# Kernel tuning notes

Hardware: AMD Instinct MI355X
Metric: run time of the kernel (lower is better)

## Reference

```python
import jax, jax.numpy as jnp
import numpy as np
from jax import lax

D_MODEL = 768
N_LAYER = 4
VOCAB = 50280  # 50277 padded to multiple of 8
D_INNER = 2 * D_MODEL
D_STATE = 16
D_CONV = 4
DT_RANK = 48  # ceil(768/16)
EPS = 1e-5


def setup_inputs() -> dict:
    key = jax.random.key(0)
    ks = iter(jax.random.split(key, 16))
    s = 0.02
    B, L = 1, 1024
    inp = {
        "input_ids": jax.random.randint(next(ks), (B, L), 0, 50277, dtype=jnp.int64).astype(jnp.int32),
        "embedding": jax.random.normal(next(ks), (VOCAB, D_MODEL), jnp.float32) * s,
        "in_proj_w": jax.random.normal(next(ks), (N_LAYER, 2 * D_INNER, D_MODEL), jnp.float32) * s,
        "conv_w": jax.random.normal(next(ks), (N_LAYER, D_INNER, 1, D_CONV), jnp.float32) * s,
        "conv_b": jnp.zeros((N_LAYER, D_INNER), jnp.float32),
        "x_proj_w": jax.random.normal(next(ks), (N_LAYER, DT_RANK + 2 * D_STATE, D_INNER), jnp.float32) * s,
        "dt_proj_w": jax.random.normal(next(ks), (N_LAYER, D_INNER, DT_RANK), jnp.float32) * s,
        "dt_proj_b": jax.random.uniform(next(ks), (N_LAYER, D_INNER), jnp.float32, -4.0, -2.0),
        "A_log": jnp.log(jnp.broadcast_to(jnp.arange(1, D_STATE + 1, dtype=jnp.float32), (N_LAYER, D_INNER, D_STATE))),
        "D_param": jnp.ones((N_LAYER, D_INNER), jnp.float32),
        "out_proj_w": jax.random.normal(next(ks), (N_LAYER, D_MODEL, D_INNER), jnp.float32) * s,
        "norm_w": jnp.ones((N_LAYER, D_MODEL), jnp.float32),
        "norm_f_w": jnp.ones((D_MODEL,), jnp.float32),
    }
    return inp


def rmsnorm(x, w):
    var = jnp.mean(jnp.square(x), axis=-1, keepdims=True)
    return x * lax.rsqrt(var + EPS) * w


def silu(x):
    return x * jax.nn.sigmoid(x)


def mamba_mixer(h, in_w, cw, cb, xw, dtw, dtb, A_log, Dp, ow):
    B, L, _ = h.shape
    xz = jnp.einsum("bld,ed->ble", h, in_w)          # [B,L,2*d_inner]
    x, z = jnp.split(xz, 2, axis=-1)
    # causal depthwise conv1d over length
    xc = lax.conv_general_dilated(
        x.transpose(0, 2, 1), cw, (1,), [(D_CONV - 1, 0)],
        dimension_numbers=("NCH", "OIH", "NCH"), feature_group_count=D_INNER,
    ).transpose(0, 2, 1) + cb                          # [B,L,d_inner]
    xc = silu(xc)
    dbl = jnp.einsum("bld,ed->ble", xc, xw)            # [B,L,R+2N]
    dt = jax.nn.softplus(jnp.einsum("blr,dr->bld", dbl[..., :DT_RANK], dtw) + dtb)
    Bm = dbl[..., DT_RANK:DT_RANK + D_STATE]           # [B,L,N]
    Cm = dbl[..., DT_RANK + D_STATE:]                  # [B,L,N]
    A = -jnp.exp(A_log)                                # [d_inner,N]
    dA = jnp.exp(dt[..., None] * A)                    # [B,L,d_inner,N]
    dBx = dt[..., None] * Bm[:, :, None, :] * xc[..., None]

    def step(s, inp):
        a, b, c = inp
        s = a * s + b
        y = jnp.einsum("bdn,bn->bd", s, c)
        return s, y

    s0 = jnp.zeros((B, D_INNER, D_STATE), h.dtype)
    _, ys = lax.scan(step, s0, (dA.transpose(1, 0, 2, 3), dBx.transpose(1, 0, 2, 3), Cm.transpose(1, 0, 2)))
    y = ys.transpose(1, 0, 2) + xc * Dp                # [B,L,d_inner]
    y = y * silu(z)
    return jnp.einsum("ble,de->bld", y, ow)


def reference(input_ids, embedding, in_proj_w, conv_w, conv_b, x_proj_w,
              dt_proj_w, dt_proj_b, A_log, D_param, out_proj_w, norm_w, norm_f_w):
    h = embedding[input_ids]                           # [B,L,D]
    for i in range(N_LAYER):
        h = h + mamba_mixer(rmsnorm(h, norm_w[i]), in_proj_w[i], conv_w[i], conv_b[i],
                            x_proj_w[i], dt_proj_w[i], dt_proj_b[i], A_log[i],
                            D_param[i], out_proj_w[i])
    h = rmsnorm(h, norm_f_w)
    logits = jnp.einsum("bld,vd->blv", h, embedding)   # tied lm_head
    return logits
```

## Files before the change

### kernel.cpp

```cpp
#include <hip/hip_runtime.h>
#include <cstdint>
#include <cstddef>

#define N_LAYER 4
#define VOCABSZ 50280
#define VOCABPAD 50304
#define DMODEL 768
#define DINNER 1536
#define DSTATE 16
#define DTRANK 48
#define SEQL 1024
#define HPSTRIDE (SEQL * DMODEL)
#define XPSTRIDE (SEQL * 80)

typedef __bf16 bf16x8 __attribute__((ext_vector_type(8)));
typedef unsigned short us8 __attribute__((ext_vector_type(8)));
typedef float f32x4 __attribute__((ext_vector_type(4)));

__device__ __forceinline__ unsigned short f2bf(float f) {
    unsigned int u = __builtin_bit_cast(unsigned int, f);
    u = (u + 0x7FFFu + ((u >> 16) & 1u)) >> 16;
    return (unsigned short)u;
}

__device__ __forceinline__ void glds16(const unsigned short* g, unsigned short* l) {
    __builtin_amdgcn_global_load_lds(
        (const __attribute__((address_space(1))) void*)g,
        (__attribute__((address_space(3))) void*)l, 16, 0, 0);
}

__device__ __forceinline__ void cvt8(const float* s, unsigned short* d) {
    const float4* s4 = (const float4*)s;
    float4 a = s4[0], b = s4[1];
    us8 o = { f2bf(a.x), f2bf(a.y), f2bf(a.z), f2bf(a.w),
              f2bf(b.x), f2bf(b.y), f2bf(b.z), f2bf(b.w) };
    *(us8*)d = o;
}

__global__ __launch_bounds__(256) void cvt_bf16_kernel(
    const float* __restrict__ src, unsigned short* __restrict__ dst, int n8)
{
    int i = blockIdx.x * 256 + threadIdx.x;
    if (i >= n8) return;
    cvt8(src + (size_t)i * 8, dst + (size_t)i * 8);
}

__global__ __launch_bounds__(256) void cvt3_kernel(
    const float* __restrict__ s0, unsigned short* __restrict__ d0, int n0,
    const float* __restrict__ s1, unsigned short* __restrict__ d1, int n1,
    const float* __restrict__ s2, unsigned short* __restrict__ d2, int n2)
{
    int i = blockIdx.x * 256 + threadIdx.x;
    const float* s; unsigned short* d; int j = i;
    if (j < n0) { s = s0; d = d0; }
    else {
        j -= n0;
        if (j < n1) { s = s1; d = d1; }
        else {
            j -= n1;
            if (j >= n2) return;
            s = s2; d = d2;
        }
    }
    cvt8(s + (size_t)j * 8, d + (size_t)j * 8);
}

__global__ __launch_bounds__(256) void cvt_xw_kernel(
    const float* __restrict__ xw, unsigned short* __restrict__ xwB)
{
    int g = blockIdx.x * 256 + threadIdx.x;
    if (g >= N_LAYER * 128 * 192) return;
    int row = g / 192;
    int c8  = g % 192;
    int layer = row >> 7;
    int r = row & 127;
    us8 o;
    if (r < 80) {
        const float4* s = (const float4*)(xw + ((size_t)(layer * 80 + r) * DINNER) + c8 * 8);
        float4 a = s[0], b = s[1];
        o = (us8){ f2bf(a.x), f2bf(a.y), f2bf(a.z), f2bf(a.w),
                   f2bf(b.x), f2bf(b.y), f2bf(b.z), f2bf(b.w) };
    } else {
        o = (us8){0, 0, 0, 0, 0, 0, 0, 0};
    }
    *(us8*)(xwB + (size_t)row * DINNER + c8 * 8) = o;
}

__device__ __forceinline__ void gemm_compute32(
    const unsigned short* sAbuf, const unsigned short* sBbuf,
    int wm, int wn, int frs, f32x4 (&acc)[4][4])
{
    bf16x8 af[4], bfr[4];
#pragma unroll
    for (int t = 0; t < 4; ++t) {
        af[t]  = __builtin_bit_cast(bf16x8, *(const us8*)&sAbuf[(wm + t * 16) * 32 + frs]);
        bfr[t] = __builtin_bit_cast(bf16x8, *(const us8*)&sBbuf[(wn + t * 16) * 32 + frs]);
    }
#pragma unroll
    for (int mt = 0; mt < 4; ++mt)
#pragma unroll
        for (int nt = 0; nt < 4; ++nt)
            acc[mt][nt] = __builtin_amdgcn_mfma_f32_16x16x32_bf16(
                af[mt], bfr[nt], acc[mt][nt], 0, 0, 0);
}

__device__ __forceinline__ void gemm_core(
    const unsigned short* __restrict__ A, const unsigned short* __restrict__ B,
    float* __restrict__ C, int N, int Kstride, int Klen, int bm, int bn)
{
    __shared__ unsigned short sA0[128 * 32];
    __shared__ unsigned short sA1[128 * 32];
    __shared__ unsigned short sB0[128 * 32];
    __shared__ unsigned short sB1[128 * 32];

    const int tid  = threadIdx.x;
    const int lane = tid & 63;
    const int wave = tid >> 6;
    const int wm = (wave & 1) * 64;
    const int wn = (wave >> 1) * 64;

    const int scol = ((tid & 3) ^ ((tid >> 3) & 3)) * 8;
    const unsigned short* Ag0 = A + (size_t)(bm + (tid >> 2)) * Kstride + scol;
    const unsigned short* Ag1 = Ag0 + (size_t)64 * Kstride;
    const unsigned short* Bg0 = B + (size_t)(bn + (tid >> 2)) * Kstride + scol;
    const unsigned short* Bg1 = Bg0 + (size_t)64 * Kstride;
    unsigned short* lA0a = sA0 + tid * 8;  unsigned short* lA0b = lA0a + 2048;
    unsigned short* lA1a = sA1 + tid * 8;  unsigned short* lA1b = lA1a + 2048;
    unsigned short* lB0a = sB0 + tid * 8;  unsigned short* lB0b = lB0a + 2048;
    unsigned short* lB1a = sB1 + tid * 8;  unsigned short* lB1b = lB1a + 2048;

    f32x4 acc[4][4];
#pragma unroll
    for (int i = 0; i < 4; ++i)
#pragma unroll
        for (int j = 0; j < 4; ++j) acc[i][j] = (f32x4){0.f, 0.f, 0.f, 0.f};

    const int frs = (lane & 15) * 32 + (((lane >> 4) ^ ((lane >> 1) & 3))) * 8;

    glds16(Ag0, lA0a); glds16(Ag1, lA0b);
    glds16(Bg0, lB0a); glds16(Bg1, lB0b);
    Ag0 += 32; Ag1 += 32; Bg0 += 32; Bg1 += 32;
    __syncthreads();

    for (int k0 = 0; k0 < Klen; k0 += 64) {
        glds16(Ag0, lA1a); glds16(Ag1, lA1b);
        glds16(Bg0, lB1a); glds16(Bg1, lB1b);
        Ag0 += 32; Ag1 += 32; Bg0 += 32; Bg1 += 32;
        gemm_compute32(sA0, sB0, wm, wn, frs, acc);
        __syncthreads();

        if (k0 + 64 < Klen) {
            glds16(Ag0, lA0a); glds16(Ag1, lA0b);
            glds16(Bg0, lB0a); glds16(Bg1, lB0b);
            Ag0 += 32; Ag1 += 32; Bg0 += 32; Bg1 += 32;
        }
        gemm_compute32(sA1, sB1, wm, wn, frs, acc);
        __syncthreads();
    }

    const int cn = lane & 15;
    const int cm = (lane >> 4) * 4;
#pragma unroll
    for (int mt = 0; mt < 4; ++mt) {
#pragma unroll
        for (int nt = 0; nt < 4; ++nt) {
            int n = bn + wn + nt * 16 + cn;
            if (n < N) {
#pragma unroll
                for (int r = 0; r < 4; ++r) {
                    int m = bm + wm + mt * 16 + cm + r;
                    C[(size_t)m * N + n] = acc[mt][nt][r];
                }
            }
        }
    }
}

__device__ __forceinline__ void swz_mn(int bid, int grid, int& bm, int& bn)
{
    int cpx = grid >> 3;
    int swz = (bid & 7) * cpx + (bid >> 3);
    bm = (swz & 7) << 7;
    bn = (swz >> 3) << 7;
}

__global__ __launch_bounds__(256) void gemm_in_kernel(
    const unsigned short* __restrict__ A, const unsigned short* __restrict__ B,
    float* __restrict__ C, int N, int K)
{ int bm, bn; swz_mn(blockIdx.x, gridDim.x, bm, bn); gemm_core(A, B, C, N, K, K, bm, bn); }

__global__ __launch_bounds__(256) void gemm_xprojk_kernel(
    const unsigned short* __restrict__ A, const unsigned short* __restrict__ B,
    float* __restrict__ xpp)
{
    int split = blockIdx.x >> 3;
    int bm = (blockIdx.x & 7) << 7;
    int kbase = split * 192;
    gemm_core(A + kbase, B + kbase, xpp + (size_t)split * XPSTRIDE,
              80, DINNER, 192, bm, 0);
}

__global__ __launch_bounds__(256) void xred_kernel(
    const float* __restrict__ xpp, float* __restrict__ dbl)
{
    int i = blockIdx.x * 256 + threadIdx.x;
    if (i >= XPSTRIDE / 4) return;
    const f32x4* p = (const f32x4*)xpp + i;
    f32x4 s = p[0];
#pragma unroll
    for (int k = 1; k < 8; ++k) s += p[(size_t)k * (XPSTRIDE / 4)];
    ((f32x4*)dbl)[i] = s;
}

__global__ __launch_bounds__(256) void gemm_outp_kernel(
    const unsigned short* __restrict__ A, const unsigned short* __restrict__ B,
    float* __restrict__ hp, int N, int Kstride, int Klen)
{
    int bid = blockIdx.x;
    int split = bid / 48;
    int r = bid - split * 48;
    int swz = (r & 7) * 6 + (r >> 3);
    int bm = (swz & 7) << 7;
    int bn = (swz >> 3) << 7;
    int kbase = split * Klen;
    gemm_core(A + kbase, B + kbase, hp + (size_t)split * HPSTRIDE,
              N, Kstride, Klen, bm, bn);
}

__global__ __launch_bounds__(256) void gemm_logits_kernel(
    const unsigned short* __restrict__ A, const unsigned short* __restrict__ B,
    float* __restrict__ C, int N, int K)
{
    __shared__ unsigned short sA[128 * 32];
    __shared__ unsigned short sB[128 * 32];

    const int tid  = threadIdx.x;
    const int lane = tid & 63;
    const int wave = tid >> 6;
    const int wm = (wave & 1) * 64;
    const int wn = (wave >> 1) * 64;
    int bm, bn;
    swz_mn(blockIdx.x, gridDim.x, bm, bn);

    const int scol = ((tid & 3) ^ ((tid >> 3) & 3)) * 8;
    const unsigned short* Ag0 = A + (size_t)(bm + (tid >> 2)) * K + scol;
    const unsigned short* Ag1 = Ag0 + (size_t)64 * K;
    const unsigned short* Bg0 = B + (size_t)(bn + (tid >> 2)) * K + scol;
    const unsigned short* Bg1 = Bg0 + (size_t)64 * K;
    unsigned short* lA0 = sA + tid * 8;
    unsigned short* lA1 = lA0 + 2048;
    unsigned short* lB0 = sB + tid * 8;
    unsigned short* lB1 = lB0 + 2048;

    f32x4 acc[4][4];
#pragma unroll
    for (int i = 0; i < 4; ++i)
#pragma unroll
        for (int j = 0; j < 4; ++j) acc[i][j] = (f32x4){0.f, 0.f, 0.f, 0.f};

    const int frs = (lane & 15) * 32 + (((lane >> 4) ^ ((lane >> 1) & 3))) * 8;

    for (int k0 = 0; k0 < K; k0 += 32) {
        __syncthreads();
        glds16(Ag0, lA0);
        glds16(Ag1, lA1);
        glds16(Bg0, lB0);
        glds16(Bg1, lB1);
        Ag0 += 32; Ag1 += 32; Bg0 += 32; Bg1 += 32;
        __syncthreads();
        gemm_compute32(sA, sB, wm, wn, frs, acc);
    }

    const int cn = lane & 15;
    const int cm = (lane >> 4) * 4;
#pragma unroll
    for (int mt = 0; mt < 4; ++mt) {
#pragma unroll
        for (int nt = 0; nt < 4; ++nt) {
            int n = bn + wn + nt * 16 + cn;
            if (n < N) {
#pragma unroll
                for (int r = 0; r < 4; ++r) {
                    int m = bm + wm + mt * 16 + cm + r;
                    C[(size_t)m * N + n] = acc[mt][nt][r];
                }
            }
        }
    }
}

template <int ADD>
__global__ __launch_bounds__(256) void gemm_fb_kernel(
    const float* __restrict__ A, const float* __restrict__ B,
    const float* __restrict__ ADDSRC, float* __restrict__ C,
    int N, int K)
{
    __shared__ unsigned short sA[128 * 40];
    __shared__ unsigned short sB[128 * 40];
    const int tid  = threadIdx.x;
    const int lane = tid & 63;
    const int wave = tid >> 6;
    const int wm = (wave & 1) * 64;
    const int wn = (wave >> 1) * 64;
    const int bm = blockIdx.y * 128;
    const int bn = blockIdx.x * 128;
    const int srow = tid >> 1;
    const int scol = (tid & 1) * 16;
    const float* Ap = A + (size_t)(bm + srow) * K + scol;
    const int brow  = bn + srow;
    const bool bvalid = brow < N;
    const float* Bp = B + (size_t)(bvalid ? brow : 0) * K + scol;
    f32x4 acc[4][4];
#pragma unroll
    for (int i = 0; i < 4; ++i)
#pragma unroll
        for (int j = 0; j < 4; ++j) acc[i][j] = (f32x4){0.f, 0.f, 0.f, 0.f};
    unsigned short* sAp = &sA[srow * 40 + scol];
    unsigned short* sBp = &sB[srow * 40 + scol];
    const int fr = (lane & 15) * 40 + (lane >> 4) * 8;
    for (int k0 = 0; k0 < K; k0 += 32) {
        float4 a0 = *(const float4*)(Ap + k0);
        float4 a1 = *(const float4*)(Ap + k0 + 4);
        float4 a2 = *(const float4*)(Ap + k0 + 8);
        float4 a3 = *(const float4*)(Ap + k0 + 12);
        float4 b0, b1, b2, b3;
        if (bvalid) {
            b0 = *(const float4*)(Bp + k0);
            b1 = *(const float4*)(Bp + k0 + 4);
            b2 = *(const float4*)(Bp + k0 + 8);
            b3 = *(const float4*)(Bp + k0 + 12);
        } else {
            b0 = make_float4(0.f, 0.f, 0.f, 0.f);
            b1 = b0; b2 = b0; b3 = b0;
        }
        __syncthreads();
        us8 va0 = { f2bf(a0.x), f2bf(a0.y), f2bf(a0.z), f2bf(a0.w),
                    f2bf(a1.x), f2bf(a1.y), f2bf(a1.z), f2bf(a1.w) };
        us8 va1 = { f2bf(a2.x), f2bf(a2.y), f2bf(a2.z), f2bf(a2.w),
                    f2bf(a3.x), f2bf(a3.y), f2bf(a3.z), f2bf(a3.w) };
        us8 vb0 = { f2bf(b0.x), f2bf(b0.y), f2bf(b0.z), f2bf(b0.w),
                    f2bf(b1.x), f2bf(b1.y), f2bf(b1.z), f2bf(b1.w) };
        us8 vb1 = { f2bf(b2.x), f2bf(b2.y), f2bf(b2.z), f2bf(b2.w),
                    f2bf(b3.x), f2bf(b3.y), f2bf(b3.z), f2bf(b3.w) };
        *(us8*)(sAp)     = va0;
        *(us8*)(sAp + 8) = va1;
        *(us8*)(sBp)     = vb0;
        *(us8*)(sBp + 8) = vb1;
        __syncthreads();
        bf16x8 af[4], bfr[4];
#pragma unroll
        for (int t = 0; t < 4; ++t) {
            af[t]  = __builtin_bit_cast(bf16x8, *(const us8*)&sA[wm * 40 + t * 640 + fr]);
            bfr[t] = __builtin_bit_cast(bf16x8, *(const us8*)&sB[wn * 40 + t * 640 + fr]);
        }
#pragma unroll
        for (int mt = 0; mt < 4; ++mt)
#pragma unroll
            for (int nt = 0; nt < 4; ++nt)
                acc[mt][nt] = __builtin_amdgcn_mfma_f32_16x16x32_bf16(
                    af[mt], bfr[nt], acc[mt][nt], 0, 0, 0);
    }
    const int cn = lane & 15;
    const int cm = (lane >> 4) * 4;
#pragma unroll
    for (int mt = 0; mt < 4; ++mt) {
#pragma unroll
        for (int nt = 0; nt < 4; ++nt) {
            int n = bn + wn + nt * 16 + cn;
            if (n < N) {
#pragma unroll
                for (int r = 0; r < 4; ++r) {
                    int m = bm + wm + mt * 16 + cm + r;
                    size_t idx = (size_t)m * N + n;
                    float v = acc[mt][nt][r];
                    if constexpr (ADD) v += ADDSRC[idx];
                    C[idx] = v;
                }
            }
        }
    }
}

__global__ __launch_bounds__(256) void embed_kernel(
    const int* __restrict__ ids, const float* __restrict__ emb, float* __restrict__ h)
{
    int l = blockIdx.x;
    int id = ids[l];
    const float* src = emb + (size_t)id * DMODEL;
    for (int d = threadIdx.x; d < DMODEL; d += 256) h[(size_t)l * DMODEL + d] = src[d];
}

template <typename OT>
__global__ __launch_bounds__(256) void rmsnorm_kernel(
    const float* __restrict__ x, const float* __restrict__ w,
    OT* __restrict__ out, int D)
{
    int l = blockIdx.x;
    const float* xr = x + (size_t)l * D;
    float ss = 0.f;
    for (int d = threadIdx.x; d < D; d += 256) { float v = xr[d]; ss += v * v; }
#pragma unroll
    for (int off = 32; off > 0; off >>= 1) ss += __shfl_down(ss, off, 64);
    __shared__ float red[4];
    __shared__ float invs;
    if ((threadIdx.x & 63) == 0) red[threadIdx.x >> 6] = ss;
    __syncthreads();
    if (threadIdx.x == 0)
        invs = rsqrtf((red[0] + red[1] + red[2] + red[3]) / (float)D + 1e-5f);
    __syncthreads();
    float inv = invs;
    for (int d = threadIdx.x; d < D; d += 256) {
        float v = xr[d] * inv * w[d];
        if constexpr (sizeof(OT) == 2) out[(size_t)l * D + d] = f2bf(v);
        else                           out[(size_t)l * D + d] = v;
    }
}

__global__ __launch_bounds__(256) void rmsnorm_acc_kernel(
    float* __restrict__ h, const float* __restrict__ hp,
    const float* __restrict__ w, unsigned short* __restrict__ out)
{
    int l = blockIdx.x;
    const size_t base = (size_t)l * DMODEL;
    __shared__ float row[DMODEL];
    float ss = 0.f;
    for (int d = threadIdx.x; d < DMODEL; d += 256) {
        float v = h[base + d]
                + hp[base + d]
                + hp[base + d + (size_t)HPSTRIDE]
                + hp[base + d + (size_t)2 * HPSTRIDE]
                + hp[base + d + (size_t)3 * HPSTRIDE];
        row[d] = v;
        h[base + d] = v;
        ss += v * v;
    }
#pragma unroll
    for (int off = 32; off > 0; off >>= 1) ss += __shfl_down(ss, off, 64);
    __shared__ float red[4];
    __shared__ float invs;
    if ((threadIdx.x & 63) == 0) red[threadIdx.x >> 6] = ss;
    __syncthreads();
    if (threadIdx.x == 0)
        invs = rsqrtf((red[0] + red[1] + red[2] + red[3]) / (float)DMODEL + 1e-5f);
    __syncthreads();
    float inv = invs;
    for (int d = threadIdx.x; d < DMODEL; d += 256)
        out[base + d] = f2bf(row[d] * inv * w[d]);
}

__global__ __launch_bounds__(256) void conv_silu_kernel(
    const float* __restrict__ xz, const float* __restrict__ cw,
    const float* __restrict__ cb, float* __restrict__ xc,
    unsigned short* __restrict__ xcB)
{
    int l = blockIdx.x / 6;
    int d = (blockIdx.x % 6) * 256 + threadIdx.x;
    float w0 = cw[d * 4], w1 = cw[d * 4 + 1], w2 = cw[d * 4 + 2], w3 = cw[d * 4 + 3];
    float acc = cb[d];
    if (l >= 3) acc += xz[(size_t)(l - 3) * 3072 + d] * w0;
    if (l >= 2) acc += xz[(size_t)(l - 2) * 3072 + d] * w1;
    if (l >= 1) acc += xz[(size_t)(l - 1) * 3072 + d] * w2;
    acc += xz[(size_t)l * 3072 + d] * w3;
    float sig = 1.f / (1.f + __expf(-acc));
    float v = acc * sig;
    size_t idx = (size_t)l * DINNER + d;
    xc[idx]  = v;
    xcB[idx] = f2bf(v);
}

__global__ __launch_bounds__(256) void xproj_kernel(
    const float* __restrict__ xc, const float* __restrict__ xw, float* __restrict__ dbl)
{
    int l = blockIdx.x;
    __shared__ float sx[DINNER];
    for (int d = threadIdx.x; d < DINNER; d += 256) sx[d] = xc[(size_t)l * DINNER + d];
    __syncthreads();
    int wave = threadIdx.x >> 6, lane = threadIdx.x & 63;
    for (int e = wave * 20; e < wave * 20 + 20; ++e) {
        const float* wr = xw + (size_t)e * DINNER;
        float s = 0.f;
        for (int d = lane; d < DINNER; d += 64) s += sx[d] * wr[d];
#pragma unroll
        for (int off = 32; off > 0; off >>= 1) s += __shfl_down(s, off, 64);
        if (lane == 0) dbl[l * 80 + e] = s;
    }
}

__global__ __launch_bounds__(256) void dtproj_kernel(
    const float* __restrict__ dbl, const float* __restrict__ dtw,
    const float* __restrict__ dtb, float* __restrict__ dt)
{
    int l = blockIdx.x / 6;
    int e = (blockIdx.x % 6) * 256 + threadIdx.x;
    __shared__ float sd[48];
    if (threadIdx.x < 48) sd[threadIdx.x] = dbl[l * 80 + threadIdx.x];
    __syncthreads();
    float a = dtb[e];
    const float4* wr = (const float4*)(dtw + (size_t)e * 48);
#pragma unroll
    for (int q = 0; q < 12; ++q) {
        float4 w4 = wr[q];
        a += sd[q * 4] * w4.x + sd[q * 4 + 1] * w4.y + sd[q * 4 + 2] * w4.z + sd[q * 4 + 3] * w4.w;
    }
    dt[(size_t)l * DINNER + e] = (a > 20.f) ? a : log1pf(__expf(a));
}

template <typename OT>
__global__ __launch_bounds__(64) void scan_kernel(
    const float* __restrict__ dt, const float* __restrict__ dbl,
    const float* __restrict__ xc, const float* __restrict__ xz,
    const float* __restrict__ alog, const float* __restrict__ dpar,
    OT* __restrict__ yf)
{
    int d0 = blockIdx.x * 4;
    int lane = threadIdx.x;
    int n = lane & 15;
    int dloc = lane >> 4;
    int d = d0 + dloc;
    float A = -__expf(alog[d * 16 + n]);
    float Dq[4];
#pragma unroll
    for (int q = 0; q < 4; ++q) Dq[q] = dpar[d0 + q];

    __shared__ float sdt[64][4];
    __shared__ float sxc[64][4];
    __shared__ float sz[64][4];
    __shared__ float sB[64][16];
    __shared__ float sC[64][16];
    __shared__ float pp[4][64][17];

    float s = 0.f;
    for (int c0 = 0; c0 < SEQL; c0 += 64) {
        int l = c0 + lane;
        *(float4*)&sdt[lane][0] = *(const float4*)&dt[(size_t)l * DINNER + d0];
        *(float4*)&sxc[lane][0] = *(const float4*)&xc[(size_t)l * DINNER + d0];
        *(float4*)&sz[lane][0]  = *(const float4*)&xz[(size_t)l * 3072 + DINNER + d0];
#pragma unroll
        for (int q = 0; q < 4; ++q) {
            *(float4*)&sB[lane][q * 4] = *(const float4*)&dbl[l * 80 + 48 + q * 4];
            *(float4*)&sC[lane][q * 4] = *(const float4*)&dbl[l * 80 + 64 + q * 4];
        }
        __syncthreads();
#pragma unroll 4
        for (int j = 0; j < 64; ++j) {
            float dtv = sdt[j][dloc];
            float xv  = sxc[j][dloc];
            float a = __expf(dtv * A);
            s = fmaf(a, s, dtv * sB[j][n] * xv);
            pp[dloc][j][n] = s * sC[j][n];
        }
        __syncthreads();
#pragma unroll
        for (int q = 0; q < 4; ++q) {
            float accv = 0.f;
#pragma unroll
            for (int nn = 0; nn < 16; ++nn) accv += pp[q][lane][nn];
            float xv = sxc[lane][q];
            float zv = sz[lane][q];
            float sig = 1.f / (1.f + __expf(-zv));
            float v = (accv + xv * Dq[q]) * (zv * sig);
            if constexpr (sizeof(OT) == 2) yf[(size_t)(c0 + lane) * DINNER + d0 + q] = f2bf(v);
            else                           yf[(size_t)(c0 + lane) * DINNER + d0 + q] = v;
        }
        __syncthreads();
    }
}

__global__ __launch_bounds__(64) void scan_fused_kernel(
    const float* __restrict__ dbl, const float* __restrict__ xc,
    const float* __restrict__ xz, const float* __restrict__ dtw,
    const float* __restrict__ dtb, const float* __restrict__ alog,
    const float* __restrict__ dpar, unsigned short* __restrict__ yf)
{
    int d0 = blockIdx.x * 4;
    int lane = threadIdx.x;
    int n = lane & 15;
    int dloc = lane >> 4;
    int d = d0 + dloc;
    float A = -__expf(alog[d * 16 + n]);
    float Dq[4], dtbq[4];
#pragma unroll
    for (int q = 0; q < 4; ++q) { Dq[q] = dpar[d0 + q]; dtbq[q] = dtb[d0 + q]; }

    __shared__ float swt[4][48];
    for (int t = lane; t < 192; t += 64)
        swt[t / 48][t % 48] = dtw[(size_t)(d0 + t / 48) * 48 + t % 48];

    __shared__ float sdt[64][4];
    __shared__ float sxc[64][4];
    __shared__ float sz[64][4];
    __shared__ float sB[64][16];
    __shared__ float sC[64][16];
    __shared__ float pp[4][64][17];

    float4 rxc, rz, rdb[12], rB[4], rC[4];

    auto loadchunk = [&](int c0) {
        int l = c0 + lane;
        rxc = *(const float4*)&xc[(size_t)l * DINNER + d0];
        rz  = *(const float4*)&xz[(size_t)l * 3072 + DINNER + d0];
#pragma unroll
        for (int q4 = 0; q4 < 12; ++q4)
            rdb[q4] = *(const float4*)&dbl[l * 80 + q4 * 4];
#pragma unroll
        for (int q = 0; q < 4; ++q) {
            rB[q] = *(const float4*)&dbl[l * 80 + 48 + q * 4];
            rC[q] = *(const float4*)&dbl[l * 80 + 64 + q * 4];
        }
    };

    loadchunk(0);
    __syncthreads();

    float s = 0.f;
    for (int c0 = 0; c0 < SEQL; c0 += 64) {
        *(float4*)&sxc[lane][0] = rxc;
        *(float4*)&sz[lane][0]  = rz;
#pragma unroll
        for (int q = 0; q < 4; ++q) {
            *(float4*)&sB[lane][q * 4] = rB[q];
            *(float4*)&sC[lane][q * 4] = rC[q];
        }
#pragma unroll
        for (int q = 0; q < 4; ++q) {
            float a = dtbq[q];
#pragma unroll
            for (int q4 = 0; q4 < 12; ++q4) {
                float4 w4 = *(const float4*)&swt[q][q4 * 4];
                a += rdb[q4].x * w4.x + rdb[q4].y * w4.y + rdb[q4].z * w4.z + rdb[q4].w * w4.w;
            }
            sdt[lane][q] = (a > 20.f) ? a : log1pf(__expf(a));
        }
        float excv[4] = { rxc.x, rxc.y, rxc.z, rxc.w };
        float ezv[4]  = { rz.x,  rz.y,  rz.z,  rz.w  };
        __syncthreads();

        if (c0 + 64 < SEQL) loadchunk(c0 + 64);

#pragma unroll 4
        for (int j = 0; j < 64; ++j) {
            float dtv = sdt[j][dloc];
            float xv  = sxc[j][dloc];
            float a = __expf(dtv * A);
            s = fmaf(a, s, dtv * sB[j][n] * xv);
            pp[dloc][j][n] = s * sC[j][n];
        }
        __syncthreads();
#pragma unroll
        for (int q = 0; q < 4; ++q) {
            float accv = 0.f;
#pragma unroll
            for (int nn = 0; nn < 16; ++nn) accv += pp[q][lane][nn];
            float zv = ezv[q];
            float sig = 1.f / (1.f + __expf(-zv));
            float v = (accv + excv[q] * Dq[q]) * (zv * sig);
            yf[(size_t)(c0 + lane) * DINNER + d0 + q] = f2bf(v);
        }
        __syncthreads();
    }
}

extern "C" void kernel_launch(void* const* d_in, const int* in_sizes, int n_in,
                              void* d_out, int out_size, void* d_ws, size_t ws_size,
                              hipStream_t stream)
{
    const int*   ids  = (const int*)d_in[0];
    const float* emb  = (const float*)d_in[1];
    const float* inw  = (const float*)d_in[2];
    const float* cw   = (const float*)d_in[3];
    const float* cb   = (const float*)d_in[4];
    const float* xw   = (const float*)d_in[5];
    const float* dtw  = (const float*)d_in[6];
    const float* dtb  = (const float*)d_in[7];
    const float* alog = (const float*)d_in[8];
    const float* dpar = (const float*)d_in[9];
    const float* ow   = (const float*)d_in[10];
    const float* nw   = (const float*)d_in[11];
    const float* nfw  = (const float*)d_in[12];
    float* out = (float*)d_out;

    const size_t MAIN_WS = 138936320ull;

    if (ws_size >= MAIN_WS) {
        char* p = (char*)d_ws;
        float* h    = (float*)p;                 p += (size_t)SEQL * DMODEL * 4;
        float* xz   = (float*)p;                 p += (size_t)SEQL * 3072 * 4;
        float* xc   = (float*)p;                 p += (size_t)SEQL * DINNER * 4;
        float* dbl  = (float*)p;                 p += (size_t)SEQL * 80 * 4;
        float* dt_unused = (float*)p;            p += (size_t)SEQL * DINNER * 4;
        unsigned short* xnB  = (unsigned short*)p; p += (size_t)SEQL * DMODEL * 2;
        unsigned short* yfB  = (unsigned short*)p; p += (size_t)SEQL * DINNER * 2;
        unsigned short* embB = (unsigned short*)p; p += (size_t)VOCABPAD * DMODEL * 2;
        unsigned short* inwB = (unsigned short*)p; p += (size_t)N_LAYER * 3072 * DMODEL * 2;
        unsigned short* owB  = (unsigned short*)p; p += (size_t)N_LAYER * DMODEL * DINNER * 2;
        (void)dt_unused;

        unsigned short* xwB = (unsigned short*)out;
        unsigned short* xcB = xwB + (size_t)N_LAYER * 128 * DINNER;
        float* hp  = (float*)(xcB + (size_t)SEQL * DINNER);
        float* xpp = hp + (size_t)4 * HPSTRIDE;

        const int n0 = VOCABSZ * DMODEL / 8;
        const int n1 = N_LAYER * 3072 * DMODEL / 8;
        const int n2 = N_LAYER * DMODEL * DINNER / 8;
        cvt3_kernel<<<(n0 + n1 + n2 + 255) / 256, 256, 0, stream>>>(
            emb, embB, n0, inw, inwB, n1, ow, owB, n2);
        cvt_xw_kernel<<<(N_LAYER * 128 * 192 + 255) / 256, 256, 0, stream>>>(xw, xwB);

        embed_kernel<<<SEQL, 256, 0, stream>>>(ids, emb, h);

        for (int i = 0; i < N_LAYER; ++i) {
            if (i == 0)
                rmsnorm_kernel<unsigned short><<<SEQL, 256, 0, stream>>>(
                    h, nw, xnB, DMODEL);
            else
                rmsnorm_acc_kernel<<<SEQL, 256, 0, stream>>>(
                    h, hp, nw + (size_t)i * DMODEL, xnB);
            gemm_in_kernel<<<8 * (3072 / 128), 256, 0, stream>>>(
                xnB, inwB + (size_t)i * 3072 * DMODEL, xz, 3072, DMODEL);
            conv_silu_kernel<<<SEQL * 6, 256, 0, stream>>>(
                xz, cw + (size_t)i * DINNER * 4, cb + (size_t)i * DINNER, xc, xcB);
            gemm_xprojk_kernel<<<64, 256, 0, stream>>>(
                xcB, xwB + (size_t)i * 128 * DINNER, xpp);
            xred_kernel<<<(XPSTRIDE / 4 + 255) / 256, 256, 0, stream>>>(xpp, dbl);
            scan_fused_kernel<<<DINNER / 4, 64, 0, stream>>>(
                dbl, xc, xz, dtw + (size_t)i * DINNER * DTRANK,
                dtb + (size_t)i * DINNER, alog + (size_t)i * DINNER * DSTATE,
                dpar + (size_t)i * DINNER, yfB);
            gemm_outp_kernel<<<4 * 48, 256, 0, stream>>>(
                yfB, owB + (size_t)i * DMODEL * DINNER, hp, DMODEL, DINNER, DINNER / 4);
        }

        rmsnorm_acc_kernel<<<SEQL, 256, 0, stream>>>(h, hp, nfw, xnB);
        gemm_logits_kernel<<<8 * ((VOCABSZ + 127) / 128), 256, 0, stream>>>(
            xnB, embB, out, VOCABSZ, DMODEL);
    } else {
        float* h   = (float*)d_ws;
        float* xn  = h  + (size_t)SEQL * DMODEL;
        float* xz  = xn + (size_t)SEQL * DMODEL;
        float* xc  = xz + (size_t)SEQL * 3072;
        float* dbl = xc + (size_t)SEQL * DINNER;
        float* dt  = dbl + (size_t)SEQL * 80;
        float* yf  = dt + (size_t)SEQL * DINNER;
        unsigned short* xcB = (unsigned short*)out;

        embed_kernel<<<SEQL, 256, 0, stream>>>(ids, emb, h);
        for (int i = 0; i < N_LAYER; ++i) {
            rmsnorm_kernel<float><<<SEQL, 256, 0, stream>>>(h, nw + (size_t)i * DMODEL, xn, DMODEL);
            gemm_fb_kernel<0><<<dim3(3072 / 128, SEQL / 128), 256, 0, stream>>>(
                xn, inw + (size_t)i * 3072 * DMODEL, nullptr, xz, 3072, DMODEL);
            conv_silu_kernel<<<SEQL * 6, 256, 0, stream>>>(
                xz, cw + (size_t)i * DINNER * 4, cb + (size_t)i * DINNER, xc, xcB);
            xproj_kernel<<<SEQL, 256, 0, stream>>>(xc, xw + (size_t)i * 80 * DINNER, dbl);
            dtproj_kernel<<<SEQL * 6, 256, 0, stream>>>(
                dbl, dtw + (size_t)i * DINNER * DTRANK, dtb + (size_t)i * DINNER, dt);
            scan_kernel<float><<<DINNER / 4, 64, 0, stream>>>(
                dt, dbl, xc, xz, alog + (size_t)i * DINNER * DSTATE, dpar + (size_t)i * DINNER, yf);
            gemm_fb_kernel<1><<<dim3(DMODEL / 128, SEQL / 128), 256, 0, stream>>>(
                yf, ow + (size_t)i * DMODEL * DINNER, h, h, DMODEL, DINNER);
        }
        rmsnorm_kernel<float><<<SEQL, 256, 0, stream>>>(h, nfw, xn, DMODEL);
        gemm_fb_kernel<0><<<dim3((VOCABSZ + 127) / 128, SEQL / 128), 256, 0, stream>>>(
            xn, emb, nullptr, out, VOCABSZ, DMODEL);
    }
}
```

Measured before the change: 1.105 ms.

## Split selective scan into chunked three-pass parallel scan over sequence segments

Replaces the single sequential-over-length scan kernel (384 blocks of 64 threads) with a three-phase chunked scan. Pass A computes each of 16 segments' local final state and decay product, pass B stitches the initial states serially across segments, and pass C reruns each segment from its correct initial state to produce outputs. This raises parallelism 16x so the GPU fills, at the cost of recomputing dt and the recurrence twice, two extra launches, and scratch buffers placed in the output region.

```diff
diff --git a/kernel.cpp b/kernel.cpp
--- a/kernel.cpp
+++ b/kernel.cpp
@@ -12,6 +12,8 @@
 #define SEQL 1024
 #define HPSTRIDE (SEQL * DMODEL)
 #define XPSTRIDE (SEQL * 80)
+#define NSEG 16
+#define DN (DINNER * DSTATE)
 
 typedef __bf16 bf16x8 __attribute__((ext_vector_type(8)));
 typedef unsigned short us8 __attribute__((ext_vector_type(8)));
@@ -566,13 +568,98 @@
     }
 }
 
-__global__ __launch_bounds__(64) void scan_fused_kernel(
+__global__ __launch_bounds__(64) void scan_partA_kernel(
+    const float* __restrict__ dbl, const float* __restrict__ xc,
+    const float* __restrict__ dtw, const float* __restrict__ dtb,
+    const float* __restrict__ alog,
+    float* __restrict__ spart, float* __restrict__ aprod)
+{
+    int bid  = blockIdx.x;
+    int seg  = bid / (DINNER / 4);
+    int dblk = bid % (DINNER / 4);
+    int d0 = dblk * 4;
+    int lane = threadIdx.x;
+    int n = lane & 15;
+    int dloc = lane >> 4;
+    int d = d0 + dloc;
+    float A = -__expf(alog[d * 16 + n]);
+    float dtbq[4];
+#pragma unroll
+    for (int q = 0; q < 4; ++q) dtbq[q] = dtb[d0 + q];
+
+    __shared__ float swt[4][48];
+    for (int t = lane; t < 192; t += 64)
+        swt[t / 48][t % 48] = dtw[(size_t)(d0 + t / 48) * 48 + t % 48];
+
+    __shared__ float sdt[64][4];
+    __shared__ float sxc[64][4];
+    __shared__ float sB[64][16];
+
+    int l = seg * 64 + lane;
+    float4 rxc = *(const float4*)&xc[(size_t)l * DINNER + d0];
+    float4 rdb[12];
+#pragma unroll
+    for (int q4 = 0; q4 < 12; ++q4)
+        rdb[q4] = *(const float4*)&dbl[l * 80 + q4 * 4];
+    float4 rB[4];
+#pragma unroll
+    for (int q = 0; q < 4; ++q) rB[q] = *(const float4*)&dbl[l * 80 + 48 + q * 4];
+
+    __syncthreads();
+    *(float4*)&sxc[lane][0] = rxc;
+#pragma unroll
+    for (int q = 0; q < 4; ++q) *(float4*)&sB[lane][q * 4] = rB[q];
+#pragma unroll
+    for (int q = 0; q < 4; ++q) {
+        float a = dtbq[q];
+#pragma unroll
+        for (int q4 = 0; q4 < 12; ++q4) {
+            float4 w4 = *(const float4*)&swt[q][q4 * 4];
+            a += rdb[q4].x * w4.x + rdb[q4].y * w4.y + rdb[q4].z * w4.z + rdb[q4].w * w4.w;
+        }
+        sdt[lane][q] = (a > 20.f) ? a : log1pf(__expf(a));
+    }
+    __syncthreads();
+
+    float s = 0.f, ap = 1.f;
+#pragma unroll 4
+    for (int j = 0; j < 64; ++j) {
+        float dtv = sdt[j][dloc];
+        float xv  = sxc[j][dloc];
+        float a = __expf(dtv * A);
+        s = fmaf(a, s, dtv * sB[j][n] * xv);
+        ap *= a;
+    }
+    size_t o = (size_t)seg * DN + (size_t)d * 16 + n;
+    spart[o] = s;
+    aprod[o] = ap;
+}
+
+__global__ __launch_bounds__(256) void scan_fixB_kernel(
+    const float* __restrict__ spart, const float* __restrict__ aprod,
+    float* __restrict__ sinit)
+{
+    int i = blockIdx.x * 256 + threadIdx.x;
+    if (i >= DN) return;
+    float s = 0.f;
+#pragma unroll
+    for (int k = 0; k < NSEG; ++k) {
+        sinit[(size_t)k * DN + i] = s;
+        s = aprod[(size_t)k * DN + i] * s + spart[(size_t)k * DN + i];
+    }
+}
+
+__global__ __launch_bounds__(64) void scan_outC_kernel(
     const float* __restrict__ dbl, const float* __restrict__ xc,
     const float* __restrict__ xz, const float* __restrict__ dtw,
     const float* __restrict__ dtb, const float* __restrict__ alog,
-    const float* __restrict__ dpar, unsigned short* __restrict__ yf)
-{
-    int d0 = blockIdx.x * 4;
+    const float* __restrict__ dpar, const float* __restrict__ sinit,
+    unsigned short* __restrict__ yf)
+{
+    int bid  = blockIdx.x;
+    int seg  = bid / (DINNER / 4);
+    int dblk = bid % (DINNER / 4);
+    int d0 = dblk * 4;
     int lane = threadIdx.x;
     int n = lane & 15;
     int dloc = lane >> 4;
@@ -593,70 +680,61 @@
     __shared__ float sC[64][16];
     __shared__ float pp[4][64][17];
 
-    float4 rxc, rz, rdb[12], rB[4], rC[4];
-
-    auto loadchunk = [&](int c0) {
-        int l = c0 + lane;
-        rxc = *(const float4*)&xc[(size_t)l * DINNER + d0];
-        rz  = *(const float4*)&xz[(size_t)l * 3072 + DINNER + d0];
-#pragma unroll
-        for (int q4 = 0; q4 < 12; ++q4)
-            rdb[q4] = *(const float4*)&dbl[l * 80 + q4 * 4];
-#pragma unroll
-        for (int q = 0; q < 4; ++q) {
-            rB[q] = *(const float4*)&dbl[l * 80 + 48 + q * 4];
-            rC[q] = *(const float4*)&dbl[l * 80 + 64 + q * 4];
-        }
-    };
-
-    loadchunk(0);
-    __syncthreads();
-
-    float s = 0.f;
-    for (int c0 = 0; c0 < SEQL; c0 += 64) {
-        *(float4*)&sxc[lane][0] = rxc;
-        *(float4*)&sz[lane][0]  = rz;
-#pragma unroll
-        for (int q = 0; q < 4; ++q) {
-            *(float4*)&sB[lane][q * 4] = rB[q];
-            *(float4*)&sC[lane][q * 4] = rC[q];
-        }
-#pragma unroll
-        for (int q = 0; q < 4; ++q) {
-            float a = dtbq[q];
-#pragma unroll
-            for (int q4 = 0; q4 < 12; ++q4) {
-                float4 w4 = *(const float4*)&swt[q][q4 * 4];
-                a += rdb[q4].x * w4.x + rdb[q4].y * w4.y + rdb[q4].z * w4.z + rdb[q4].w * w4.w;
-            }
-            sdt[lane][q] = (a > 20.f) ? a : log1pf(__expf(a));
-        }
-        float excv[4] = { rxc.x, rxc.y, rxc.z, rxc.w };
-        float ezv[4]  = { rz.x,  rz.y,  rz.z,  rz.w  };
-        __syncthreads();
-
-        if (c0 + 64 < SEQL) loadchunk(c0 + 64);
+    int l = seg * 64 + lane;
+    float4 rxc = *(const float4*)&xc[(size_t)l * DINNER + d0];
+    float4 rz  = *(const float4*)&xz[(size_t)l * 3072 + DINNER + d0];
+    float4 rdb[12];
+#pragma unroll
+    for (int q4 = 0; q4 < 12; ++q4)
+        rdb[q4] = *(const float4*)&dbl[l * 80 + q4 * 4];
+    float4 rB[4], rC[4];
+#pragma unroll
+    for (int q = 0; q < 4; ++q) {
+        rB[q] = *(const float4*)&dbl[l * 80 + 48 + q * 4];
+        rC[q] = *(const float4*)&dbl[l * 80 + 64 + q * 4];
+    }
+    float s = sinit[(size_t)seg * DN + (size_t)d * 16 + n];
+
+    __syncthreads();
+    *(float4*)&sxc[lane][0] = rxc;
+    *(float4*)&sz[lane][0]  = rz;
+#pragma unroll
+    for (int q = 0; q < 4; ++q) {
+        *(float4*)&sB[lane][q * 4] = rB[q];
+        *(float4*)&sC[lane][q * 4] = rC[q];
+    }
+#pragma unroll
+    for (int q = 0; q < 4; ++q) {
+        float a = dtbq[q];
+#pragma unroll
+        for (int q4 = 0; q4 < 12; ++q4) {
+            float4 w4 = *(const float4*)&swt[q][q4 * 4];
+            a += rdb[q4].x * w4.x + rdb[q4].y * w4.y + rdb[q4].z * w4.z + rdb[q4].w * w4.w;
+        }
+        sdt[lane][q] = (a > 20.f) ? a : log1pf(__expf(a));
+    }
+    float excv[4] = { rxc.x, rxc.y, rxc.z, rxc.w };
+    float ezv[4]  = { rz.x,  rz.y,  rz.z,  rz.w  };
+    __syncthreads();
 
 #pragma unroll 4
-        for (int j = 0; j < 64; ++j) {
-            float dtv = sdt[j][dloc];
-            float xv  = sxc[j][dloc];
-            float a = __expf(dtv * A);
-            s = fmaf(a, s, dtv * sB[j][n] * xv);
-            pp[dloc][j][n] = s * sC[j][n];
-        }
-        __syncthreads();
-#pragma unroll
-        for (int q = 0; q < 4; ++q) {
-            float accv = 0.f;
-#pragma unroll
-            for (int nn = 0; nn < 16; ++nn) accv += pp[q][lane][nn];
-            float zv = ezv[q];
-            float sig = 1.f / (1.f + __expf(-zv));
-            float v = (accv + excv[q] * Dq[q]) * (zv * sig);
-            yf[(size_t)(c0 + lane) * DINNER + d0 + q] = f2bf(v);
-        }
-        __syncthreads();
+    for (int j = 0; j < 64; ++j) {
+        float dtv = sdt[j][dloc];
+        float xv  = sxc[j][dloc];
+        float a = __expf(dtv * A);
+        s = fmaf(a, s, dtv * sB[j][n] * xv);
+        pp[dloc][j][n] = s * sC[j][n];
+    }
+    __syncthreads();
+#pragma unroll
+    for (int q = 0; q < 4; ++q) {
+        float accv = 0.f;
+#pragma unroll
+        for (int nn = 0; nn < 16; ++nn) accv += pp[q][lane][nn];
+        float zv = ezv[q];
+        float sig = 1.f / (1.f + __expf(-zv));
+        float v = (accv + excv[q] * Dq[q]) * (zv * sig);
+        yf[(size_t)(seg * 64 + lane) * DINNER + d0 + q] = f2bf(v);
     }
 }
 
@@ -697,8 +775,11 @@
 
         unsigned short* xwB = (unsigned short*)out;
         unsigned short* xcB = xwB + (size_t)N_LAYER * 128 * DINNER;
-        float* hp  = (float*)(xcB + (size_t)SEQL * DINNER);
-        float* xpp = hp + (size_t)4 * HPSTRIDE;
+        float* hp    = (float*)(xcB + (size_t)SEQL * DINNER);
+        float* xpp   = hp + (size_t)4 * HPSTRIDE;
+        float* spart = xpp + (size_t)8 * XPSTRIDE;
+        float* aprod = spart + (size_t)NSEG * DN;
+        float* sinit = aprod + (size_t)NSEG * DN;
 
         const int n0 = VOCABSZ * DMODEL / 8;
         const int n1 = N_LAYER * 3072 * DMODEL / 8;
@@ -723,10 +804,16 @@
             gemm_xprojk_kernel<<<64, 256, 0, stream>>>(
                 xcB, xwB + (size_t)i * 128 * DINNER, xpp);
             xred_kernel<<<(XPSTRIDE / 4 + 255) / 256, 256, 0, stream>>>(xpp, dbl);
-            scan_fused_kernel<<<DINNER / 4, 64, 0, stream>>>(
+            scan_partA_kernel<<<NSEG * (DINNER / 4), 64, 0, stream>>>(
+                dbl, xc, dtw + (size_t)i * DINNER * DTRANK,
+                dtb + (size_t)i * DINNER, alog + (size_t)i * DINNER * DSTATE,
+                spart, aprod);
+            scan_fixB_kernel<<<(DN + 255) / 256, 256, 0, stream>>>(
+                spart, aprod, sinit);
+            scan_outC_kernel<<<NSEG * (DINNER / 4), 64, 0, stream>>>(
                 dbl, xc, xz, dtw + (size_t)i * DINNER * DTRANK,
                 dtb + (size_t)i * DINNER, alog + (size_t)i * DINNER * DSTATE,
-                dpar + (size_t)i * DINNER, yfB);
+                dpar + (size_t)i * DINNER, sinit, yfB);
             gemm_outp_kernel<<<4 * 48, 256, 0, stream>>>(
                 yfB, owB + (size_t)i * DMODEL * DINNER, hp, DMODEL, DINNER, DINNER / 4);
         }
```

Result: faster. 1.056 ms (-4.5%).
